# Kernel optimization log

Measured on AMD Instinct MI355X. Metric: run time of the kernel, lower is better.

Reference implementation:

```python
import jax, jax.numpy as jnp
import numpy as np

N_HEAD = 16
D_HEAD = 64
D_MODEL = 1024
LN_EPS = 1e-5


def layer_norm(x, gamma, beta):
    mu = jnp.mean(x, axis=-1, keepdims=True)
    var = jnp.mean((x - mu) ** 2, axis=-1, keepdims=True)
    return (x - mu) * jax.lax.rsqrt(var + LN_EPS) * gamma + beta


def setup_inputs() -> dict:
    key = jax.random.key(0)
    ks = jax.random.split(key, 6)
    B, T = 2, 2048
    inp = jax.random.normal(ks[0], (B, T, D_MODEL), dtype=jnp.float32)
    # qkv_net: Linear(d_model, 3*n_head*d_head)
    W_qkv = jax.random.normal(ks[1], (3 * N_HEAD * D_HEAD, D_MODEL), dtype=jnp.float32) * (D_MODEL ** -0.5)
    b_qkv = jax.random.normal(ks[2], (3 * N_HEAD * D_HEAD,), dtype=jnp.float32) * 0.02
    # o_net: Linear(n_head*d_head, d_model, bias=False)
    W_o = jax.random.normal(ks[3], (D_MODEL, N_HEAD * D_HEAD), dtype=jnp.float32) * ((N_HEAD * D_HEAD) ** -0.5)
    gamma = jnp.ones((D_MODEL,), dtype=jnp.float32)
    beta = jnp.zeros((D_MODEL,), dtype=jnp.float32)
    return {"inp": inp, "W_qkv": W_qkv, "b_qkv": b_qkv, "W_o": W_o, "gamma": gamma, "beta": beta}


def reference(inp, W_qkv, b_qkv, W_o, gamma, beta):
    B, T, D = inp.shape
    H, dh = N_HEAD, D_HEAD
    scale = 1.0 / (dh ** 0.5)

    qkv = inp @ W_qkv.T + b_qkv                      # (B, T, 3*H*dh)
    head_q, head_k, head_v = jnp.split(qkv, 3, axis=2)
    # (B, T, H, dh) -> (B, H, T, dh)
    q = head_q.reshape(B, T, H, dh).transpose(0, 2, 1, 3)
    k = head_k.reshape(B, T, H, dh).transpose(0, 2, 1, 3)
    v = head_v.reshape(B, T, H, dh).transpose(0, 2, 1, 3)

    attn_score = jnp.einsum('bhqd,bhkd->bhqk', q, k) * scale  # (B, H, T, T)
    attn_prob = jax.nn.softmax(attn_score, axis=-1)           # dropatt is identity in eval
    attn_vec = jnp.einsum('bhqk,bhkd->bhqd', attn_prob, v)    # (B, H, T, dh)

    # Faithful to original: (B*H, T, dh) batch-major buffer is VIEWED as (H, B, T, dh)
    attn_vec = attn_vec.reshape(H, B, T, dh)
    attn_vec = attn_vec.transpose(1, 2, 0, 3).reshape(B, T, H * dh)

    attn_out = attn_vec @ W_o.T                                # dropout identity in eval
    return layer_norm(inp + attn_out, gamma, beta)
```

## Files before the change

### kernel.cpp

```cpp
#include <hip/hip_runtime.h>
#include <hip/hip_bf16.h>
#include <stdint.h>

typedef __bf16 bf16_t;
typedef __bf16 bf16x8 __attribute__((ext_vector_type(8)));
typedef __bf16 bf16x4 __attribute__((ext_vector_type(4)));
typedef __bf16 bf16x2 __attribute__((ext_vector_type(2)));
typedef float floatx4 __attribute__((ext_vector_type(4)));

#define QSCALE 0.180336879f

#if __has_builtin(__builtin_amdgcn_cvt_pk_bf16_f32)
#define HAS_PK_BF16 1
#endif

__device__ static inline void gll16(const void* g, void* l) {
    __builtin_amdgcn_global_load_lds((const __attribute__((address_space(1))) void*)g,
                                     (__attribute__((address_space(3))) void*)l, 16, 0, 0);
}

__device__ static inline bf16x8 pack8(const float* p) {
    bf16x8 o;
#ifdef HAS_PK_BF16
#pragma unroll
    for (int j = 0; j < 4; j++) {
        bf16x2 t2 = __builtin_amdgcn_cvt_pk_bf16_f32(p[2 * j], p[2 * j + 1]);
        o[2 * j] = t2[0]; o[2 * j + 1] = t2[1];
    }
#else
#pragma unroll
    for (int j = 0; j < 8; j++) o[j] = (bf16_t)p[j];
#endif
    return o;
}

__global__ __launch_bounds__(256) void cvt_all(const float* __restrict__ inp,
                                               const float* __restrict__ wqkv,
                                               const float* __restrict__ wo,
                                               bf16_t* __restrict__ o_inp,
                                               bf16_t* __restrict__ o_wqkv,
                                               bf16_t* __restrict__ o_wo) {
    int blk = blockIdx.x;
    const float* src;
    bf16_t* dst;
    if (blk < 4096)      { src = inp;  dst = o_inp; }
    else if (blk < 7168) { src = wqkv; dst = o_wqkv; blk -= 4096; }
    else                 { src = wo;   dst = o_wo;   blk -= 7168; }
    int i = blk * 256 + threadIdx.x;
    float4 v = ((const float4*)src)[i];
    float p[4] = {v.x, v.y, v.z, v.w};
    bf16x4 o;
#ifdef HAS_PK_BF16
    bf16x2 t0 = __builtin_amdgcn_cvt_pk_bf16_f32(p[0], p[1]);
    bf16x2 t1 = __builtin_amdgcn_cvt_pk_bf16_f32(p[2], p[3]);
    o[0] = t0[0]; o[1] = t0[1]; o[2] = t1[0]; o[3] = t1[1];
#else
    o[0] = (bf16_t)p[0]; o[1] = (bf16_t)p[1]; o[2] = (bf16_t)p[2]; o[3] = (bf16_t)p[3];
#endif
    ((bf16x4*)dst)[i] = o;
}

__global__ __launch_bounds__(256, 3)
void gemm_qkv(const bf16_t* __restrict__ A, const bf16_t* __restrict__ Bw,
              const float* __restrict__ bias,
              bf16_t* __restrict__ qk, bf16_t* __restrict__ vT) {
    constexpr int K = 1024;
    __shared__ bf16_t lA[3][128 * 32];
    __shared__ bf16_t lB[3][128 * 32];
    const int tid  = threadIdx.x;
    const int lane = tid & 63, wave = tid >> 6;
    const int quad = lane >> 4, l16 = lane & 15;
    const int wy = wave >> 1, wx = wave & 1;

    const int L  = blockIdx.y * 24 + blockIdx.x;
    const int nL = (L & 7) * 96 + (L >> 3);
    const int bm = (nL / 24) * 128, bn = (nL % 24) * 128;

    const int c0 = tid, c1 = tid + 256;
    const int k0 = ((c0 & 3) ^ ((c0 >> 3) & 3)) * 8;
    const int k1 = ((c1 & 3) ^ ((c1 >> 3) & 3)) * 8;
    const bf16_t* Ap0 = A + (size_t)(bm + (c0 >> 2)) * K + k0;
    const bf16_t* Ap1 = A + (size_t)(bm + (c1 >> 2)) * K + k1;
    const bf16_t* Bp0 = Bw + (size_t)(bn + (c0 >> 2)) * K + k0;
    const bf16_t* Bp1 = Bw + (size_t)(bn + (c1 >> 2)) * K + k1;
    const int d0 = (wave * 64) * 8;
    const int d1 = (256 + wave * 64) * 8;

    const int sq8 = (quad ^ ((l16 >> 1) & 3)) * 8;

    floatx4 acc[4][4] = {};

    gll16(Ap0, &lA[0][d0]); gll16(Ap1, &lA[0][d1]);
    gll16(Bp0, &lB[0][d0]); gll16(Bp1, &lB[0][d1]);
    gll16(Ap0 + 32, &lA[1][d0]); gll16(Ap1 + 32, &lA[1][d1]);
    gll16(Bp0 + 32, &lB[1][d0]); gll16(Bp1 + 32, &lB[1][d1]);

    int cur = 0;
    for (int it = 0; it < 32; ++it) {
        if (it < 30) {
            const int kt = (it + 2) * 32;
            const int nb = cur >= 1 ? cur - 1 : 2;
            gll16(Ap0 + kt, &lA[nb][d0]); gll16(Ap1 + kt, &lA[nb][d1]);
            gll16(Bp0 + kt, &lB[nb][d0]); gll16(Bp1 + kt, &lB[nb][d1]);
            asm volatile("s_waitcnt vmcnt(8)" ::: "memory");
        } else if (it == 30) {
            asm volatile("s_waitcnt vmcnt(4)" ::: "memory");
        } else {
            asm volatile("s_waitcnt vmcnt(0)" ::: "memory");
        }
        __builtin_amdgcn_s_barrier();
        __builtin_amdgcn_sched_barrier(0);

        bf16x8 af[4], bfr[4];
#pragma unroll
        for (int i = 0; i < 4; i++) {
            af[i]  = *(const bf16x8*)(&lA[cur][(wy * 64 + i * 16 + l16) * 32 + sq8]);
            bfr[i] = *(const bf16x8*)(&lB[cur][(wx * 64 + i * 16 + l16) * 32 + sq8]);
        }
#pragma unroll
        for (int i = 0; i < 4; i++)
#pragma unroll
            for (int j = 0; j < 4; j++)
                acc[i][j] = __builtin_amdgcn_mfma_f32_16x16x32_bf16(af[i], bfr[j], acc[i][j], 0, 0, 0);

        __builtin_amdgcn_sched_barrier(0);
        __builtin_amdgcn_s_barrier();
        cur = cur < 2 ? cur + 1 : 0;
    }

    const bool is_v = (bn >= 2048);
#pragma unroll
    for (int j = 0; j < 4; j++) {
        const int n = bn + wx * 64 + j * 16 + l16;
        const float bv = bias[n];
        const bool isq = (n < 1024);
#pragma unroll
        for (int i = 0; i < 4; i++) {
            const int mbase = bm + wy * 64 + i * 16 + quad * 4;
            if (!is_v) {
#pragma unroll
                for (int r = 0; r < 4; r++) {
                    float c = acc[i][j][r] + bv;
                    if (isq) c *= QSCALE;
                    qk[(size_t)(mbase + r) * 2048 + n] = (bf16_t)c;
                }
            } else {
                const int nn = n - 2048;
                const int b  = mbase >> 11;
                const int t  = mbase & 2047;
                const int vrow = b * 1024 + nn;
                const int pcol = (t & ~31) | (((t >> 2) & 3) << 3) | (((t >> 4) & 1) << 2);
                bf16x4 pack;
#pragma unroll
                for (int r = 0; r < 4; r++) pack[r] = (bf16_t)(acc[i][j][r] + bv);
                *(bf16x4*)(vT + (size_t)vrow * 2048 + pcol) = pack;
            }
        }
    }
}

__global__ __launch_bounds__(256, 4)
void attn_kernel(const bf16_t* __restrict__ qk, const bf16_t* __restrict__ vT,
                 bf16_t* __restrict__ Opart, float* __restrict__ lpart) {
    __shared__ bf16_t Kbuf[2][64 * 64];
    __shared__ bf16_t Vbuf[2][64 * 64];
    const int tid  = threadIdx.x;
    const int lane = tid & 63, wave = tid >> 6;
    const int quad = lane >> 4, l16 = lane & 15;
    const int bid = blockIdx.x;
    const int s    = bid & 63;
    const int hl   = ((s & 7) << 2) | ((s >> 3) & 3);
    const int half = (s >> 5) & 1;
    const int qt   = bid >> 6;
    const int b = hl >> 4, h = hl & 15;
    const int kt0 = half * 1024;

    const bf16_t* Qbase = qk + (size_t)(b * 2048 + qt * 128 + wave * 32) * 2048 + h * 64;
    const bf16_t* Kbase = qk + (size_t)(b * 2048) * 2048 + 1024 + h * 64;
    const bf16_t* Vbase = vT + (size_t)(hl * 64) * 2048;

    const int srow = tid >> 2;
    const int sc8 = ((tid & 3) ^ ((tid >> 3) & 3)) * 8;
    const bf16_t* KgA = Kbase + (size_t)(kt0 + srow) * 2048 + sc8;
    const bf16_t* KgB = KgA + 32;
    const bf16_t* VgA = Vbase + (size_t)srow * 2048 + kt0 + sc8;
    const bf16_t* VgB = VgA + 32;
    const int wbase = wave * 512;

    const int xq8 = (quad ^ ((l16 >> 1) & 3)) * 8;

    bf16x8 qf[2][2];
#pragma unroll
    for (int rt = 0; rt < 2; rt++)
#pragma unroll
        for (int kc = 0; kc < 2; kc++)
            qf[rt][kc] = *(const bf16x8*)(Qbase + (size_t)(rt * 16 + l16) * 2048 + kc * 32 + quad * 8);

    floatx4 accO[2][4] = {};
    float lacc[2] = {0.f, 0.f};

    gll16(KgA, &Kbuf[0][wbase]);
    gll16(KgB, &Kbuf[0][2048 + wbase]);
    gll16(VgA, &Vbuf[0][wbase]);
    gll16(VgB, &Vbuf[0][2048 + wbase]);

    for (int it = 0; it < 16; ++it) {
        const int cur = it & 1, nxt = cur ^ 1;
        __syncthreads();
        if (it < 15) {
            const size_t ko = (size_t)(it + 1) * 64 * 2048;
            const int    vo = (it + 1) * 64;
            gll16(KgA + ko, &Kbuf[nxt][wbase]);
            gll16(KgB + ko, &Kbuf[nxt][2048 + wbase]);
            gll16(VgA + vo, &Vbuf[nxt][wbase]);
            gll16(VgB + vo, &Vbuf[nxt][2048 + wbase]);
        }
        floatx4 st[2][4] = {};
#pragma unroll
        for (int nt = 0; nt < 4; nt++) {
            bf16x8 k0 = *(const bf16x8*)&Kbuf[cur][(nt * 16 + l16) * 32 + xq8];
            bf16x8 k1 = *(const bf16x8*)&Kbuf[cur][2048 + (nt * 16 + l16) * 32 + xq8];
            st[0][nt] = __builtin_amdgcn_mfma_f32_16x16x32_bf16(k0, qf[0][0], st[0][nt], 0, 0, 0);
            st[0][nt] = __builtin_amdgcn_mfma_f32_16x16x32_bf16(k1, qf[0][1], st[0][nt], 0, 0, 0);
            st[1][nt] = __builtin_amdgcn_mfma_f32_16x16x32_bf16(k0, qf[1][0], st[1][nt], 0, 0, 0);
            st[1][nt] = __builtin_amdgcn_mfma_f32_16x16x32_bf16(k1, qf[1][1], st[1][nt], 0, 0, 0);
        }
#pragma unroll
        for (int kc2 = 0; kc2 < 2; kc2++) {
            bf16x8 vf[4];
#pragma unroll
            for (int ct = 0; ct < 4; ct++)
                vf[ct] = *(const bf16x8*)&Vbuf[cur][kc2 * 2048 + (ct * 16 + l16) * 32 + xq8];
#pragma unroll
            for (int rt = 0; rt < 2; rt++) {
                float p[8];
                float ls = 0.f;
#pragma unroll
                for (int j = 0; j < 8; j++) {
                    p[j] = __builtin_amdgcn_exp2f(st[rt][kc2 * 2 + (j >> 2)][j & 3]);
                    ls += p[j];
                }
                lacc[rt] += ls;
                bf16x8 pf = pack8(p);
#pragma unroll
                for (int ct = 0; ct < 4; ct++)
                    accO[rt][ct] = __builtin_amdgcn_mfma_f32_16x16x32_bf16(pf, vf[ct], accO[rt][ct], 0, 0, 0);
            }
        }
    }

    float lsum[2];
#pragma unroll
    for (int rt = 0; rt < 2; rt++) {
        float l = lacc[rt];
        l += __shfl_xor(l, 16);
        l += __shfl_xor(l, 32);
        lsum[rt] = l;
    }
    const int b2 = hl & 1;
    const int colb = hl >> 1;
    const int rowb = b2 * 2048 + qt * 128 + wave * 32;
    bf16_t* outb = Opart + (size_t)half * (4096 * 1024) + (size_t)rowb * 1024 + colb * 64;
#pragma unroll
    for (int rt = 0; rt < 2; rt++)
#pragma unroll
        for (int ct = 0; ct < 4; ct++)
#pragma unroll
            for (int r = 0; r < 4; r++)
                outb[(size_t)(rt * 16 + quad * 4 + r) * 1024 + ct * 16 + l16] = (bf16_t)(accO[rt][ct][r]);
    if (quad == 0) {
#pragma unroll
        for (int rt = 0; rt < 2; rt++)
            lpart[half * 65536 + (rowb + rt * 16 + l16) * 16 + colb] = lsum[rt];
    }
}

__global__ __launch_bounds__(256, 4)
void gemm_o(const bf16_t* __restrict__ Op, const float* __restrict__ lp,
            const bf16_t* __restrict__ Bw, bf16_t* __restrict__ out) {
    constexpr int K = 1024;
    __shared__ bf16_t lA[2][64 * 32];
    __shared__ bf16_t lB[2][128 * 32];
    const int tid  = threadIdx.x;
    const int lane = tid & 63, wave = tid >> 6;
    const int quad = lane >> 4, l16 = lane & 15;
    const int wy = wave >> 1, wx = wave & 1;

    const int L  = blockIdx.y * 8 + blockIdx.x;
    const int nL = (L & 7) * 64 + (L >> 3);
    const int bm = (nL >> 3) * 64, bn = (nL & 7) * 128;

    const int ca = tid;
    const int arow = bm + (ca >> 2);
    const int ak   = (ca & 3) * 8;
    const int aslot = ((ca & 3) ^ ((ca >> 3) & 3));
    const int awr   = ((ca >> 2) * 4 + aslot) * 8;
    const bf16_t* Ap0 = Op + (size_t)arow * 1024 + ak;
    const bf16_t* Ap1 = Ap0 + (size_t)4096 * 1024;
    const float*  lrow = lp + arow * 16;
    const int cb0 = tid, cb1 = tid + 256;
    const int bk0 = ((cb0 & 3) ^ ((cb0 >> 3) & 3)) * 8;
    const int bk1 = ((cb1 & 3) ^ ((cb1 >> 3) & 3)) * 8;
    const bf16_t* Bp0 = Bw + (size_t)(bn + (cb0 >> 2)) * K + bk0;
    const bf16_t* Bp1 = Bw + (size_t)(bn + (cb1 >> 2)) * K + bk1;
    const int d0 = (wave * 64) * 8;
    const int d1 = (256 + wave * 64) * 8;

    const int xq8 = (quad ^ ((l16 >> 1) & 3)) * 8;

    gll16(Bp0, &lB[0][d0]);
    gll16(Bp1, &lB[0][d1]);
    {
        bf16x8 a0 = *(const bf16x8*)(Ap0);
        bf16x8 a1 = *(const bf16x8*)(Ap1);
        const float inv = 1.0f / (lrow[ak >> 6] + lrow[65536 + (ak >> 6)]);
        float p[8];
#pragma unroll
        for (int j = 0; j < 8; j++) p[j] = ((float)a0[j] + (float)a1[j]) * inv;
        *(bf16x8*)&lA[0][awr] = pack8(p);
    }

    floatx4 acc[2][4] = {};
    for (int it = 0; it < 32; ++it) {
        const int cur = it & 1, nxt = cur ^ 1;
        __syncthreads();
        bf16x8 na0, na1;
        int kt1 = (it + 1) * 32;
        if (it < 31) {
            na0 = *(const bf16x8*)(Ap0 + kt1);
            na1 = *(const bf16x8*)(Ap1 + kt1);
            gll16(Bp0 + kt1, &lB[nxt][d0]);
            gll16(Bp1 + kt1, &lB[nxt][d1]);
        }
        bf16x8 af[2], bfr[4];
#pragma unroll
        for (int i = 0; i < 2; i++)
            af[i] = *(const bf16x8*)(&lA[cur][(wy * 32 + i * 16 + l16) * 32 + xq8]);
#pragma unroll
        for (int j = 0; j < 4; j++)
            bfr[j] = *(const bf16x8*)(&lB[cur][(wx * 64 + j * 16 + l16) * 32 + xq8]);
#pragma unroll
        for (int i = 0; i < 2; i++)
#pragma unroll
            for (int j = 0; j < 4; j++)
                acc[i][j] = __builtin_amdgcn_mfma_f32_16x16x32_bf16(af[i], bfr[j], acc[i][j], 0, 0, 0);
        if (it < 31) {
            const int cb = (kt1 + ak) >> 6;
            const float inv = 1.0f / (lrow[cb] + lrow[65536 + cb]);
            float p[8];
#pragma unroll
            for (int j = 0; j < 8; j++) p[j] = ((float)na0[j] + (float)na1[j]) * inv;
            *(bf16x8*)&lA[nxt][awr] = pack8(p);
        }
    }
#pragma unroll
    for (int j = 0; j < 4; j++) {
        const int n = bn + wx * 64 + j * 16 + l16;
#pragma unroll
        for (int i = 0; i < 2; i++) {
            const int mbase = bm + wy * 32 + i * 16 + quad * 4;
#pragma unroll
            for (int r = 0; r < 4; r++)
                out[(size_t)(mbase + r) * 1024 + n] = (bf16_t)acc[i][j][r];
        }
    }
}

__global__ __launch_bounds__(256)
void ln_kernel(const float* __restrict__ inp, const bf16_t* __restrict__ ao,
               const float* __restrict__ gamma, const float* __restrict__ beta,
               float* __restrict__ out) {
    const int row = blockIdx.x, tid = threadIdx.x;
    const int wave = tid >> 6, lane = tid & 63;
    float4 a = ((const float4*)(inp + (size_t)row * 1024))[tid];
    bf16x4 c4 = ((const bf16x4*)(ao + (size_t)row * 1024))[tid];
    float x0 = a.x + (float)c4[0], x1 = a.y + (float)c4[1];
    float x2 = a.z + (float)c4[2], x3 = a.w + (float)c4[3];
    float s = x0 + x1 + x2 + x3;
    float sq = x0 * x0 + x1 * x1 + x2 * x2 + x3 * x3;
#pragma unroll
    for (int mm = 32; mm >= 1; mm >>= 1) {
        s += __shfl_xor(s, mm);
        sq += __shfl_xor(sq, mm);
    }
    __shared__ float rs[4], rq[4];
    if (lane == 0) { rs[wave] = s; rq[wave] = sq; }
    __syncthreads();
    s = rs[0] + rs[1] + rs[2] + rs[3];
    sq = rq[0] + rq[1] + rq[2] + rq[3];
    const float mu = s * (1.0f / 1024.0f);
    const float var = sq * (1.0f / 1024.0f) - mu * mu;
    const float rstd = rsqrtf(var + 1e-5f);
    float4 g = ((const float4*)gamma)[tid], bt = ((const float4*)beta)[tid];
    float4 o;
    o.x = (x0 - mu) * rstd * g.x + bt.x;
    o.y = (x1 - mu) * rstd * g.y + bt.y;
    o.z = (x2 - mu) * rstd * g.z + bt.z;
    o.w = (x3 - mu) * rstd * g.w + bt.w;
    ((float4*)(out + (size_t)row * 1024))[tid] = o;
}

extern "C" void kernel_launch(void* const* d_in, const int* in_sizes, int n_in,
                              void* d_out, int out_size, void* d_ws, size_t ws_size,
                              hipStream_t stream) {
    const float* inp   = (const float*)d_in[0];
    const float* Wqkv  = (const float*)d_in[1];
    const float* bqkv  = (const float*)d_in[2];
    const float* Wo    = (const float*)d_in[3];
    const float* gamma = (const float*)d_in[4];
    const float* beta  = (const float*)d_in[5];
    float* out = (float*)d_out;

    char* ws = (char*)d_ws;
    bf16_t* inp_bf  = (bf16_t*)(ws);
    bf16_t* wqkv_bf = (bf16_t*)(ws + (8u << 20));
    bf16_t* wo_bf   = (bf16_t*)(ws + (14u << 20));
    bf16_t* qk_buf  = (bf16_t*)(ws + (16u << 20));
    bf16_t* vT_buf  = (bf16_t*)(ws + (32u << 20));
    bf16_t* ao_bf   = (bf16_t*)(ws + (32u << 20));
    bf16_t* opart   = (bf16_t*)(ws + (48u << 20));
    float*  lpart   = (float*)(ws);

    cvt_all<<<8192, 256, 0, stream>>>(inp, Wqkv, Wo, inp_bf, wqkv_bf, wo_bf);
    gemm_qkv<<<dim3(24, 32), 256, 0, stream>>>(inp_bf, wqkv_bf, bqkv, qk_buf, vT_buf);
    attn_kernel<<<1024, 256, 0, stream>>>(qk_buf, vT_buf, opart, lpart);
    gemm_o<<<dim3(8, 64), 256, 0, stream>>>(opart, lpart, wo_bf, ao_bf);
    ln_kernel<<<4096, 256, 0, stream>>>(inp, ao_bf, gamma, beta, out);
}
```

Baseline: 195.2 us.

## Drop split-K attention; normalize in-kernel and triple-buffer gemm_o loads

```diff
diff --git a/kernel.cpp b/kernel.cpp
--- a/kernel.cpp
+++ b/kernel.cpp
@@ -161,19 +161,17 @@
 
 __global__ __launch_bounds__(256, 4)
 void attn_kernel(const bf16_t* __restrict__ qk, const bf16_t* __restrict__ vT,
-                 bf16_t* __restrict__ Opart, float* __restrict__ lpart) {
+                 bf16_t* __restrict__ Ofin) {
     __shared__ bf16_t Kbuf[2][64 * 64];
     __shared__ bf16_t Vbuf[2][64 * 64];
     const int tid  = threadIdx.x;
     const int lane = tid & 63, wave = tid >> 6;
     const int quad = lane >> 4, l16 = lane & 15;
     const int bid = blockIdx.x;
-    const int s    = bid & 63;
+    const int s    = bid & 31;
     const int hl   = ((s & 7) << 2) | ((s >> 3) & 3);
-    const int half = (s >> 5) & 1;
-    const int qt   = bid >> 6;
+    const int qt   = bid >> 5;
     const int b = hl >> 4, h = hl & 15;
-    const int kt0 = half * 1024;
 
     const bf16_t* Qbase = qk + (size_t)(b * 2048 + qt * 128 + wave * 32) * 2048 + h * 64;
     const bf16_t* Kbase = qk + (size_t)(b * 2048) * 2048 + 1024 + h * 64;
@@ -181,9 +179,9 @@
 
     const int srow = tid >> 2;
     const int sc8 = ((tid & 3) ^ ((tid >> 3) & 3)) * 8;
-    const bf16_t* KgA = Kbase + (size_t)(kt0 + srow) * 2048 + sc8;
+    const bf16_t* KgA = Kbase + (size_t)srow * 2048 + sc8;
     const bf16_t* KgB = KgA + 32;
-    const bf16_t* VgA = Vbase + (size_t)srow * 2048 + kt0 + sc8;
+    const bf16_t* VgA = Vbase + (size_t)srow * 2048 + sc8;
     const bf16_t* VgB = VgA + 32;
     const int wbase = wave * 512;
 
@@ -204,10 +202,10 @@
     gll16(VgA, &Vbuf[0][wbase]);
     gll16(VgB, &Vbuf[0][2048 + wbase]);
 
-    for (int it = 0; it < 16; ++it) {
+    for (int it = 0; it < 32; ++it) {
         const int cur = it & 1, nxt = cur ^ 1;
         __syncthreads();
-        if (it < 15) {
+        if (it < 31) {
             const size_t ko = (size_t)(it + 1) * 64 * 2048;
             const int    vo = (it + 1) * 64;
             gll16(KgA + ko, &Kbuf[nxt][wbase]);
@@ -257,30 +255,33 @@
         l += __shfl_xor(l, 32);
         lsum[rt] = l;
     }
+    float linv[2][4];
+#pragma unroll
+    for (int rt = 0; rt < 2; rt++)
+#pragma unroll
+        for (int r = 0; r < 4; r++)
+            linv[rt][r] = 1.0f / __shfl(lsum[rt], quad * 4 + r);
+
     const int b2 = hl & 1;
     const int colb = hl >> 1;
     const int rowb = b2 * 2048 + qt * 128 + wave * 32;
-    bf16_t* outb = Opart + (size_t)half * (4096 * 1024) + (size_t)rowb * 1024 + colb * 64;
+    bf16_t* outb = Ofin + (size_t)rowb * 1024 + colb * 64;
 #pragma unroll
     for (int rt = 0; rt < 2; rt++)
 #pragma unroll
         for (int ct = 0; ct < 4; ct++)
 #pragma unroll
             for (int r = 0; r < 4; r++)
-                outb[(size_t)(rt * 16 + quad * 4 + r) * 1024 + ct * 16 + l16] = (bf16_t)(accO[rt][ct][r]);
-    if (quad == 0) {
-#pragma unroll
-        for (int rt = 0; rt < 2; rt++)
-            lpart[half * 65536 + (rowb + rt * 16 + l16) * 16 + colb] = lsum[rt];
-    }
+                outb[(size_t)(rt * 16 + quad * 4 + r) * 1024 + ct * 16 + l16] =
+                    (bf16_t)(accO[rt][ct][r] * linv[rt][r]);
 }
 
 __global__ __launch_bounds__(256, 4)
-void gemm_o(const bf16_t* __restrict__ Op, const float* __restrict__ lp,
-            const bf16_t* __restrict__ Bw, bf16_t* __restrict__ out) {
+void gemm_o(const bf16_t* __restrict__ Op, const bf16_t* __restrict__ Bw,
+            bf16_t* __restrict__ out) {
     constexpr int K = 1024;
-    __shared__ bf16_t lA[2][64 * 32];
-    __shared__ bf16_t lB[2][128 * 32];
+    __shared__ bf16_t lA[3][64 * 32];
+    __shared__ bf16_t lB[3][128 * 32];
     const int tid  = threadIdx.x;
     const int lane = tid & 63, wave = tid >> 6;
     const int quad = lane >> 4, l16 = lane & 15;
@@ -290,48 +291,41 @@
     const int nL = (L & 7) * 64 + (L >> 3);
     const int bm = (nL >> 3) * 64, bn = (nL & 7) * 128;
 
-    const int ca = tid;
-    const int arow = bm + (ca >> 2);
-    const int ak   = (ca & 3) * 8;
-    const int aslot = ((ca & 3) ^ ((ca >> 3) & 3));
-    const int awr   = ((ca >> 2) * 4 + aslot) * 8;
-    const bf16_t* Ap0 = Op + (size_t)arow * 1024 + ak;
-    const bf16_t* Ap1 = Ap0 + (size_t)4096 * 1024;
-    const float*  lrow = lp + arow * 16;
+    const int akc = ((tid & 3) ^ ((tid >> 3) & 3)) * 8;
+    const bf16_t* Ap = Op + (size_t)(bm + (tid >> 2)) * K + akc;
+    const int dA = wave * 512;
     const int cb0 = tid, cb1 = tid + 256;
     const int bk0 = ((cb0 & 3) ^ ((cb0 >> 3) & 3)) * 8;
     const int bk1 = ((cb1 & 3) ^ ((cb1 >> 3) & 3)) * 8;
     const bf16_t* Bp0 = Bw + (size_t)(bn + (cb0 >> 2)) * K + bk0;
     const bf16_t* Bp1 = Bw + (size_t)(bn + (cb1 >> 2)) * K + bk1;
-    const int d0 = (wave * 64) * 8;
-    const int d1 = (256 + wave * 64) * 8;
+    const int d0 = wave * 512;
+    const int d1 = 2048 + wave * 512;
 
     const int xq8 = (quad ^ ((l16 >> 1) & 3)) * 8;
 
-    gll16(Bp0, &lB[0][d0]);
-    gll16(Bp1, &lB[0][d1]);
-    {
-        bf16x8 a0 = *(const bf16x8*)(Ap0);
-        bf16x8 a1 = *(const bf16x8*)(Ap1);
-        const float inv = 1.0f / (lrow[ak >> 6] + lrow[65536 + (ak >> 6)]);
-        float p[8];
-#pragma unroll
-        for (int j = 0; j < 8; j++) p[j] = ((float)a0[j] + (float)a1[j]) * inv;
-        *(bf16x8*)&lA[0][awr] = pack8(p);
-    }
+    gll16(Ap, &lA[0][dA]);
+    gll16(Bp0, &lB[0][d0]); gll16(Bp1, &lB[0][d1]);
+    gll16(Ap + 32, &lA[1][dA]);
+    gll16(Bp0 + 32, &lB[1][d0]); gll16(Bp1 + 32, &lB[1][d1]);
 
     floatx4 acc[2][4] = {};
+    int cur = 0;
     for (int it = 0; it < 32; ++it) {
-        const int cur = it & 1, nxt = cur ^ 1;
-        __syncthreads();
-        bf16x8 na0, na1;
-        int kt1 = (it + 1) * 32;
-        if (it < 31) {
-            na0 = *(const bf16x8*)(Ap0 + kt1);
-            na1 = *(const bf16x8*)(Ap1 + kt1);
-            gll16(Bp0 + kt1, &lB[nxt][d0]);
-            gll16(Bp1 + kt1, &lB[nxt][d1]);
-        }
+        if (it < 30) {
+            const int kt = (it + 2) * 32;
+            const int nb = cur >= 1 ? cur - 1 : 2;
+            gll16(Ap + kt, &lA[nb][dA]);
+            gll16(Bp0 + kt, &lB[nb][d0]); gll16(Bp1 + kt, &lB[nb][d1]);
+            asm volatile("s_waitcnt vmcnt(6)" ::: "memory");
+        } else if (it == 30) {
+            asm volatile("s_waitcnt vmcnt(3)" ::: "memory");
+        } else {
+            asm volatile("s_waitcnt vmcnt(0)" ::: "memory");
+        }
+        __builtin_amdgcn_s_barrier();
+        __builtin_amdgcn_sched_barrier(0);
+
         bf16x8 af[2], bfr[4];
 #pragma unroll
         for (int i = 0; i < 2; i++)
@@ -344,14 +338,10 @@
 #pragma unroll
             for (int j = 0; j < 4; j++)
                 acc[i][j] = __builtin_amdgcn_mfma_f32_16x16x32_bf16(af[i], bfr[j], acc[i][j], 0, 0, 0);
-        if (it < 31) {
-            const int cb = (kt1 + ak) >> 6;
-            const float inv = 1.0f / (lrow[cb] + lrow[65536 + cb]);
-            float p[8];
-#pragma unroll
-            for (int j = 0; j < 8; j++) p[j] = ((float)na0[j] + (float)na1[j]) * inv;
-            *(bf16x8*)&lA[nxt][awr] = pack8(p);
-        }
+
+        __builtin_amdgcn_sched_barrier(0);
+        __builtin_amdgcn_s_barrier();
+        cur = cur < 2 ? cur + 1 : 0;
     }
 #pragma unroll
     for (int j = 0; j < 4; j++) {
@@ -418,12 +408,11 @@
     bf16_t* qk_buf  = (bf16_t*)(ws + (16u << 20));
     bf16_t* vT_buf  = (bf16_t*)(ws + (32u << 20));
     bf16_t* ao_bf   = (bf16_t*)(ws + (32u << 20));
-    bf16_t* opart   = (bf16_t*)(ws + (48u << 20));
-    float*  lpart   = (float*)(ws);
+    bf16_t* ofin    = (bf16_t*)(ws + (48u << 20));
 
     cvt_all<<<8192, 256, 0, stream>>>(inp, Wqkv, Wo, inp_bf, wqkv_bf, wo_bf);
     gemm_qkv<<<dim3(24, 32), 256, 0, stream>>>(inp_bf, wqkv_bf, bqkv, qk_buf, vT_buf);
-    attn_kernel<<<1024, 256, 0, stream>>>(qk_buf, vT_buf, opart, lpart);
-    gemm_o<<<dim3(8, 64), 256, 0, stream>>>(opart, lpart, wo_bf, ao_bf);
+    attn_kernel<<<512, 256, 0, stream>>>(qk_buf, vT_buf, ofin);
+    gemm_o<<<dim3(8, 64), 256, 0, stream>>>(ofin, wo_bf, ao_bf);
     ln_kernel<<<4096, 256, 0, stream>>>(inp, ao_bf, gamma, beta, out);
 }
```

After: 189.9 us. 2.7% less time.
